# Kernel optimization log

Measured on AMD Instinct MI355X. Metric: run time of the kernel, lower is better.

## Reference

```python
import jax, jax.numpy as jnp
import numpy as np

DIM = 512
NUM_HEADS = 8
HEAD_DIM = DIM // NUM_HEADS          # 64
KEY_DIM = int(HEAD_DIM * 0.5)        # 32
H_QKV = DIM + NUM_HEADS * KEY_DIM * 2  # 1024
SCALE = KEY_DIM ** -0.5
EPS = 1e-5


def bn(x, gamma, beta, mean, var):
    # inference-mode BatchNorm2d over channel axis 1 of NCHW
    inv = gamma / jnp.sqrt(var + EPS)
    return x * inv[None, :, None, None] + (beta - mean * inv)[None, :, None, None]


def conv1x1(x, w):
    # w: [out, in] (1x1 conv collapsed); x: NCHW
    return jnp.einsum('bchw,oc->bohw', x, w)


def dwconv3x3(x, w):
    # depthwise 3x3, 'same' padding; w: [C,1,3,3]
    return jax.lax.conv_general_dilated(
        x, w, window_strides=(1, 1), padding='SAME',
        feature_group_count=x.shape[1],
        dimension_numbers=('NCHW', 'OIHW', 'NCHW'))


def setup_inputs() -> dict:
    key = jax.random.key(0)
    ks = jax.random.split(key, 16)
    B, C, H, W = 8, DIM, 40, 40
    f = jax.random.normal
    inp = {
        'x': f(ks[0], (B, C, H, W), jnp.float32),
        'qkv_w': f(ks[1], (H_QKV, DIM), jnp.float32) * (1.0 / np.sqrt(DIM)),
        'qkv_gamma': 1.0 + 0.1 * f(ks[2], (H_QKV,), jnp.float32),
        'qkv_beta': 0.1 * f(ks[3], (H_QKV,), jnp.float32),
        'qkv_mean': 0.1 * f(ks[4], (H_QKV,), jnp.float32),
        'qkv_var': jax.random.uniform(ks[5], (H_QKV,), jnp.float32) + 0.5,
        'pe_w': f(ks[6], (DIM, 1, 3, 3), jnp.float32) * (1.0 / 3.0),
        'pe_gamma': 1.0 + 0.1 * f(ks[7], (DIM,), jnp.float32),
        'pe_beta': 0.1 * f(ks[8], (DIM,), jnp.float32),
        'pe_mean': 0.1 * f(ks[9], (DIM,), jnp.float32),
        'pe_var': jax.random.uniform(ks[10], (DIM,), jnp.float32) + 0.5,
        'proj_w': f(ks[11], (DIM, DIM), jnp.float32) * (1.0 / np.sqrt(DIM)),
        'proj_gamma': 1.0 + 0.1 * f(ks[12], (DIM,), jnp.float32),
        'proj_beta': 0.1 * f(ks[13], (DIM,), jnp.float32),
        'proj_mean': 0.1 * f(ks[14], (DIM,), jnp.float32),
        'proj_var': jax.random.uniform(ks[15], (DIM,), jnp.float32) + 0.5,
    }
    return inp


def reference(x, qkv_w, qkv_gamma, qkv_beta, qkv_mean, qkv_var,
              pe_w, pe_gamma, pe_beta, pe_mean, pe_var,
              proj_w, proj_gamma, proj_beta, proj_mean, proj_var):
    B, C, H, W = x.shape
    N = H * W
    qkv = bn(conv1x1(x, qkv_w), qkv_gamma, qkv_beta, qkv_mean, qkv_var)
    qkv = qkv.reshape(B, NUM_HEADS, KEY_DIM * 2 + HEAD_DIM, N)
    q = qkv[:, :, :KEY_DIM]                    # [B,h,kd,N]
    k = qkv[:, :, KEY_DIM:2 * KEY_DIM]         # [B,h,kd,N]
    v = qkv[:, :, 2 * KEY_DIM:]                # [B,h,hd,N]
    # attn = q^T @ k * scale -> [B,h,N,N], softmax over last dim
    attn = jnp.einsum('bhkn,bhkm->bhnm', q, k) * SCALE
    attn = jax.nn.softmax(attn, axis=-1)
    # out = v @ attn^T -> [B,h,hd,N]
    out = jnp.einsum('bhdm,bhnm->bhdn', v, attn).reshape(B, C, H, W)
    pe = bn(dwconv3x3(v.reshape(B, C, H, W), pe_w), pe_gamma, pe_beta, pe_mean, pe_var)
    y = out + pe
    y = bn(conv1x1(y, proj_w), proj_gamma, proj_beta, proj_mean, proj_var)
    return y
```

## Files before the change

kernel.cpp:

```cpp
#include <hip/hip_runtime.h>
#include <hip/hip_bf16.h>

#define EPS 1e-5f
#define SCALE 0.17677669529663687f
#define QSCALE 0.25500526817095634f

typedef __attribute__((ext_vector_type(8))) short bf16x8;
typedef __attribute__((ext_vector_type(4))) float f32x4;
typedef __attribute__((ext_vector_type(8))) unsigned short u16x8;

__device__ __forceinline__ unsigned short f2bf(float x) {
  union { float f; unsigned int u; } a; a.f = x;
  unsigned int r = a.u + 0x7FFFu + ((a.u >> 16) & 1u);
  return (unsigned short)(r >> 16);
}
__device__ __forceinline__ float bf2f(unsigned short u) {
  union { unsigned int u; float f; } a; a.u = ((unsigned int)u) << 16;
  return a.f;
}

__device__ __forceinline__ float fexp2(float x) {
#if __has_builtin(__builtin_amdgcn_exp2f)
  return __builtin_amdgcn_exp2f(x);
#else
  float r; asm("v_exp_f32 %0, %1" : "=v"(r) : "v"(x)); return r;
#endif
}

__device__ __forceinline__ void gload_lds16(const void* g, void* l) {
  __builtin_amdgcn_global_load_lds(
      (const __attribute__((address_space(1))) unsigned int*)g,
      (__attribute__((address_space(3))) unsigned int*)l, 16, 0, 0);
}

__device__ __forceinline__ unsigned int pack_bf_trunc(float a, float b) {
  return __builtin_amdgcn_perm(__float_as_uint(b), __float_as_uint(a), 0x07060302u);
}

__global__ __launch_bounds__(256) void cast_w_kernel(
    const float* __restrict__ qw, const float* __restrict__ pw,
    short* __restrict__ wq, short* __restrict__ wp) {
  int idx = blockIdx.x * 256 + threadIdx.x;
  const float4* src;
  ushort4* dst;
  if (idx < 131072) {
    src = (const float4*)qw + idx;
    dst = (ushort4*)wq + idx;
  } else {
    src = (const float4*)pw + (idx - 131072);
    dst = (ushort4*)wp + (idx - 131072);
  }
  float4 v = *src;
  ushort4 u;
  u.x = f2bf(v.x); u.y = f2bf(v.y); u.z = f2bf(v.z); u.w = f2bf(v.w);
  *dst = u;
}

__global__ __launch_bounds__(256) void transpose_cast_kernel(
    const float* __restrict__ X, short* __restrict__ XT) {
  __shared__ unsigned short T[64][72];
  const int b = blockIdx.z, c0 = blockIdx.x * 64, n0 = blockIdx.y * 64;
  const int t = threadIdx.x, nl = t & 63, w = t >> 6;
#pragma unroll
  for (int ci = 0; ci < 16; ++ci) {
    int cl = ci * 4 + w;
    T[nl][cl] = f2bf(X[((size_t)(b * 512 + c0 + cl)) * 1600 + n0 + nl]);
  }
  __syncthreads();
  const int n2 = t >> 2, cg = (t & 3) * 16;
  unsigned short* o = (unsigned short*)XT + ((size_t)(b * 1600 + n0 + n2)) * 512 + c0 + cg;
  *(u16x8*)&o[0] = *(const u16x8*)&T[n2][cg];
  *(u16x8*)&o[8] = *(const u16x8*)&T[n2][cg + 8];
}

__global__ __launch_bounds__(256) void transpose16_kernel(
    const short* __restrict__ S, short* __restrict__ D) {
  __shared__ unsigned short T[64][72];
  const int b = blockIdx.z, c0 = blockIdx.x * 64, n0 = blockIdx.y * 64;
  const int t = threadIdx.x, nl = t & 63, w = t >> 6;
  const unsigned short* Sp = (const unsigned short*)S;
#pragma unroll
  for (int ci = 0; ci < 16; ++ci) {
    int cl = ci * 4 + w;
    T[nl][cl] = Sp[((size_t)(b * 512 + c0 + cl)) * 1600 + n0 + nl];
  }
  __syncthreads();
  const int n2 = t >> 2, cg = (t & 3) * 16;
  unsigned short* o = (unsigned short*)D + ((size_t)(b * 1600 + n0 + n2)) * 512 + c0 + cg;
  *(u16x8*)&o[0] = *(const u16x8*)&T[n2][cg];
  *(u16x8*)&o[8] = *(const u16x8*)&T[n2][cg + 8];
}

__global__ __launch_bounds__(256) void qkv_mfma_kernel(
    const short* __restrict__ XT, const short* __restrict__ WQ,
    const float* __restrict__ gamma, const float* __restrict__ beta,
    const float* __restrict__ mean, const float* __restrict__ var,
    short* __restrict__ qT, short* __restrict__ kT,
    short* __restrict__ vb, short* __restrict__ vp) {
  __shared__ __align__(16) unsigned short As[128 * 32];
  __shared__ __align__(16) unsigned short Bs[128 * 32];
  __shared__ __align__(16) unsigned short Vs[128 * 68];

  const int t = threadIdx.x, w = t >> 6, lane = t & 63;
  const int quad = lane >> 4, l16 = lane & 15;
  const int wr = w >> 1, wc = w & 1;
  const int ngt = blockIdx.x, h = blockIdx.y;
  const int o0 = h * 128, ng0 = ngt * 128;

  const int srow = lane >> 2;
  const int sseg = (lane & 3) * 8;

  f32x4 acc[4][4];
#pragma unroll
  for (int mi = 0; mi < 4; ++mi)
#pragma unroll
    for (int nj = 0; nj < 4; ++nj) { acc[mi][nj][0]=0.f; acc[mi][nj][1]=0.f; acc[mi][nj][2]=0.f; acc[mi][nj][3]=0.f; }

  for (int kt = 0; kt < 16; ++kt) {
    const int c0 = kt * 32;
    if (kt) __syncthreads();
#pragma unroll
    for (int r = 0; r < 2; ++r) {
      const int row = (r * 4 + w) * 16 + srow;
      gload_lds16(WQ + (size_t)(o0 + row) * 512 + c0 + sseg, As + (r * 4 + w) * 512);
      gload_lds16(XT + (size_t)(ng0 + row) * 512 + c0 + sseg, Bs + (r * 4 + w) * 512);
    }
    __syncthreads();
    bf16x8 af[4], bfr[4];
#pragma unroll
    for (int i = 0; i < 4; ++i) {
      af[i]  = *(const bf16x8*)&As[(wr * 64 + i * 16 + l16) * 32 + quad * 8];
      bfr[i] = *(const bf16x8*)&Bs[(wc * 64 + i * 16 + l16) * 32 + quad * 8];
    }
#pragma unroll
    for (int mi = 0; mi < 4; ++mi)
#pragma unroll
      for (int nj = 0; nj < 4; ++nj)
        acc[mi][nj] = __builtin_amdgcn_mfma_f32_16x16x32_bf16(af[mi], bfr[nj], acc[mi][nj], 0, 0, 0);
  }

  const int ng_base = ng0 + wc * 64;
#pragma unroll
  for (int mi = 0; mi < 4; ++mi) {
    const int ol = wr * 64 + mi * 16 + quad * 4;
    const int ob = o0 + ol;
    float inv[4], add[4];
#pragma unroll
    for (int r = 0; r < 4; ++r) {
      inv[r] = gamma[ob + r] * rsqrtf(var[ob + r] + EPS);
      add[r] = beta[ob + r] - mean[ob + r] * inv[r];
    }
    const int region = wr * 2 + (mi >> 1);
    if (region == 0) {
      const int kk = mi * 16 + quad * 4;
#pragma unroll
      for (int nj = 0; nj < 4; ++nj) {
        int ng = ng_base + nj * 16 + l16;
        int b = ng / 1600, n = ng - b * 1600;
        ushort4 u;
        u.x = f2bf((acc[mi][nj][0] * inv[0] + add[0]) * QSCALE);
        u.y = f2bf((acc[mi][nj][1] * inv[1] + add[1]) * QSCALE);
        u.z = f2bf((acc[mi][nj][2] * inv[2] + add[2]) * QSCALE);
        u.w = f2bf((acc[mi][nj][3] * inv[3] + add[3]) * QSCALE);
        *(ushort4*)&qT[((size_t)(b * 8 + h) * 1600 + n) * 32 + kk] = u;
      }
    } else if (region == 1) {
      const int kk = (mi - 2) * 16 + quad * 4;
#pragma unroll
      for (int nj = 0; nj < 4; ++nj) {
        int ng = ng_base + nj * 16 + l16;
        int b = ng / 1600, n = ng - b * 1600;
        ushort4 u;
        u.x = f2bf(acc[mi][nj][0] * inv[0] + add[0]);
        u.y = f2bf(acc[mi][nj][1] * inv[1] + add[1]);
        u.z = f2bf(acc[mi][nj][2] * inv[2] + add[2]);
        u.w = f2bf(acc[mi][nj][3] * inv[3] + add[3]);
        *(ushort4*)&kT[((size_t)(b * 8 + h) * 1600 + n) * 32 + kk] = u;
      }
    } else {
      const int ch = h * 64 + (ol - 64);
      const int d0 = ol - 64;
#pragma unroll
      for (int nj = 0; nj < 4; ++nj) {
        int ng = ng_base + nj * 16 + l16;
        int n_local = ng - ng0;
        int b = ng / 1600, n = ng - b * 1600;
        unsigned short val[4];
#pragma unroll
        for (int r = 0; r < 4; ++r)
          val[r] = f2bf(acc[mi][nj][r] * inv[r] + add[r]);
#pragma unroll
        for (int r = 0; r < 4; ++r)
          ((unsigned short*)vb)[((size_t)(b * 512 + ch + r)) * 1600 + n] = val[r];
#pragma unroll
        for (int k = 0; k < 2; ++k) {
          unsigned int pk = (unsigned int)val[2 * k] |
                            ((unsigned int)val[2 * k + 1] << 16);
          *(unsigned int*)&Vs[n_local * 68 + d0 + 2 * k] = pk;
        }
      }
    }
  }

  __syncthreads();
#pragma unroll
  for (int cc = 0; cc < 4; ++cc) {
    const int c = cc * 256 + t;
    const int kbl = c >> 6, d = c & 63;
    const int n_gl = ng0 + kbl * 8;
    const int b = n_gl / 1600, nn = n_gl - b * 1600;
    union { unsigned short u[8]; u16x8 v; } pk;
#pragma unroll
    for (int j = 0; j < 8; ++j)
      pk.u[j] = Vs[(kbl * 8 + j) * 68 + d];
    *(u16x8*)((unsigned short*)vp +
        ((size_t)(b * 8 + h) * 200 + (nn >> 3)) * 512 + d * 8) = pk.v;
  }
}

__global__ __launch_bounds__(256) void attn_mfma_kernel(
    const short* __restrict__ qT, const short* __restrict__ kT,
    const short* __restrict__ vp, short* __restrict__ ybf) {
  const int N = 1600;
  const int t = threadIdx.x;
  const int w = t >> 6, lane = t & 63, quad = lane >> 4, l16 = lane & 15;
  const int bh = blockIdx.x, b = bh >> 3, h = bh & 7;
  const int n0w = blockIdx.y * 128 + w * 32;
  if (n0w >= 1600) return;

  const unsigned short* qTb = (const unsigned short*)qT + (size_t)bh * N * 32;
  const unsigned short* kTb = (const unsigned short*)kT + (size_t)bh * N * 32;
  const unsigned short* vpb = (const unsigned short*)vp + (size_t)bh * 102400;

  const bf16x8 qf0 = *(const bf16x8*)(qTb + (size_t)(n0w + l16) * 32 + quad * 8);
  const bf16x8 qf1 = *(const bf16x8*)(qTb + (size_t)(n0w + 16 + l16) * 32 + quad * 8);

  f32x4 acc0[4], acc1[4];
#pragma unroll
  for (int i = 0; i < 4; ++i) {
    acc0[i][0]=0.f; acc0[i][1]=0.f; acc0[i][2]=0.f; acc0[i][3]=0.f;
    acc1[i][0]=0.f; acc1[i][1]=0.f; acc1[i][2]=0.f; acc1[i][3]=0.f;
  }
  float den0 = 0.f, den1 = 0.f;
  const f32x4 zero4 = {0.f, 0.f, 0.f, 0.f};

  const int kperm = ((l16 & 12) << 1) + (l16 & 3);
  const unsigned short* kp = kTb + (size_t)kperm * 32 + quad * 8;
  const unsigned short* vq = vpb + (size_t)quad * 512 + l16 * 8;

  bf16x8 ck0 = *(const bf16x8*)kp;
  bf16x8 ck1 = *(const bf16x8*)(kp + 128);
  bf16x8 cv0 = *(const bf16x8*)(vq);
  bf16x8 cv1 = *(const bf16x8*)(vq + 128);
  bf16x8 cv2 = *(const bf16x8*)(vq + 256);
  bf16x8 cv3 = *(const bf16x8*)(vq + 384);
  bf16x8 nk0, nk1, nv0, nv1, nv2, nv3;

#define ATTN_BODY(NXT, CK0, CK1, CV0, CV1, CV2, CV3, NK0, NK1, NV0, NV1, NV2, NV3) \
  { \
    const int nx_ = (NXT) < 50 ? (NXT) : 0; \
    const unsigned short* kpn_ = kp + (size_t)nx_ * 1024; \
    const unsigned short* vqn_ = vq + (size_t)nx_ * 2048; \
    NK0 = *(const bf16x8*)kpn_; \
    NK1 = *(const bf16x8*)(kpn_ + 128); \
    NV0 = *(const bf16x8*)(vqn_); \
    NV1 = *(const bf16x8*)(vqn_ + 128); \
    NV2 = *(const bf16x8*)(vqn_ + 256); \
    NV3 = *(const bf16x8*)(vqn_ + 384); \
    f32x4 s0_ = __builtin_amdgcn_mfma_f32_16x16x32_bf16(CK0, qf0, zero4, 0, 0, 0); \
    f32x4 s1_ = __builtin_amdgcn_mfma_f32_16x16x32_bf16(CK1, qf0, zero4, 0, 0, 0); \
    f32x4 t0_ = __builtin_amdgcn_mfma_f32_16x16x32_bf16(CK0, qf1, zero4, 0, 0, 0); \
    f32x4 t1_ = __builtin_amdgcn_mfma_f32_16x16x32_bf16(CK1, qf1, zero4, 0, 0, 0); \
    float a0_ = fexp2(s0_[0]), a1_ = fexp2(s0_[1]), a2_ = fexp2(s0_[2]), a3_ = fexp2(s0_[3]); \
    float a4_ = fexp2(s1_[0]), a5_ = fexp2(s1_[1]), a6_ = fexp2(s1_[2]), a7_ = fexp2(s1_[3]); \
    float b0_ = fexp2(t0_[0]), b1_ = fexp2(t0_[1]), b2_ = fexp2(t0_[2]), b3_ = fexp2(t0_[3]); \
    float b4_ = fexp2(t1_[0]), b5_ = fexp2(t1_[1]), b6_ = fexp2(t1_[2]), b7_ = fexp2(t1_[3]); \
    den0 += ((a0_ + a1_) + (a2_ + a3_)) + ((a4_ + a5_) + (a6_ + a7_)); \
    den1 += ((b0_ + b1_) + (b2_ + b3_)) + ((b4_ + b5_) + (b6_ + b7_)); \
    union { bf16x8 v; uint4 u; } pk0_, pk1_; \
    pk0_.u.x = pack_bf_trunc(a0_, a1_); pk0_.u.y = pack_bf_trunc(a2_, a3_); \
    pk0_.u.z = pack_bf_trunc(a4_, a5_); pk0_.u.w = pack_bf_trunc(a6_, a7_); \
    pk1_.u.x = pack_bf_trunc(b0_, b1_); pk1_.u.y = pack_bf_trunc(b2_, b3_); \
    pk1_.u.z = pack_bf_trunc(b4_, b5_); pk1_.u.w = pack_bf_trunc(b6_, b7_); \
    acc0[0] = __builtin_amdgcn_mfma_f32_16x16x32_bf16(pk0_.v, CV0, acc0[0], 0, 0, 0); \
    acc1[0] = __builtin_amdgcn_mfma_f32_16x16x32_bf16(pk1_.v, CV0, acc1[0], 0, 0, 0); \
    acc0[1] = __builtin_amdgcn_mfma_f32_16x16x32_bf16(pk0_.v, CV1, acc0[1], 0, 0, 0); \
    acc1[1] = __builtin_amdgcn_mfma_f32_16x16x32_bf16(pk1_.v, CV1, acc1[1], 0, 0, 0); \
    acc0[2] = __builtin_amdgcn_mfma_f32_16x16x32_bf16(pk0_.v, CV2, acc0[2], 0, 0, 0); \
    acc1[2] = __builtin_amdgcn_mfma_f32_16x16x32_bf16(pk1_.v, CV2, acc1[2], 0, 0, 0); \
    acc0[3] = __builtin_amdgcn_mfma_f32_16x16x32_bf16(pk0_.v, CV3, acc0[3], 0, 0, 0); \
    acc1[3] = __builtin_amdgcn_mfma_f32_16x16x32_bf16(pk1_.v, CV3, acc1[3], 0, 0, 0); \
  }

#pragma unroll 1
  for (int mt2 = 0; mt2 < 25; ++mt2) {
    ATTN_BODY(2 * mt2 + 1, ck0, ck1, cv0, cv1, cv2, cv3, nk0, nk1, nv0, nv1, nv2, nv3);
    ATTN_BODY(2 * mt2 + 2, nk0, nk1, nv0, nv1, nv2, nv3, ck0, ck1, cv0, cv1, cv2, cv3);
  }
#undef ATTN_BODY

  den0 += __shfl_xor(den0, 16, 64);
  den0 += __shfl_xor(den0, 32, 64);
  den1 += __shfl_xor(den1, 16, 64);
  den1 += __shfl_xor(den1, 32, 64);
  const float rden0 = 1.f / den0;
  const float rden1 = 1.f / den1;
  float dv0[4], dv1[4];
#pragma unroll
  for (int r = 0; r < 4; ++r) {
    dv0[r] = __shfl(rden0, quad * 4 + r, 64);
    dv1[r] = __shfl(rden1, quad * 4 + r, 64);
  }

  unsigned short* yb = (unsigned short*)ybf + ((size_t)b * 512 + h * 64) * N;
#pragma unroll
  for (int i = 0; i < 4; ++i) {
    const size_t rowo = (size_t)(i * 16 + l16) * N;
    ushort4 o4;
    o4.x = f2bf(acc0[i][0] * dv0[0]);
    o4.y = f2bf(acc0[i][1] * dv0[1]);
    o4.z = f2bf(acc0[i][2] * dv0[2]);
    o4.w = f2bf(acc0[i][3] * dv0[3]);
    *(ushort4*)&yb[rowo + n0w + quad * 4] = o4;
    o4.x = f2bf(acc1[i][0] * dv1[0]);
    o4.y = f2bf(acc1[i][1] * dv1[1]);
    o4.z = f2bf(acc1[i][2] * dv1[2]);
    o4.w = f2bf(acc1[i][3] * dv1[3]);
    *(ushort4*)&yb[rowo + n0w + 16 + quad * 4] = o4;
  }
}

__global__ __launch_bounds__(256) void pe_kernel(
    const short* __restrict__ Ybf, const short* __restrict__ VB,
    const float* __restrict__ pw,
    const float* __restrict__ gamma, const float* __restrict__ beta,
    const float* __restrict__ mean, const float* __restrict__ var,
    short* __restrict__ YB) {
  __shared__ __align__(16) unsigned short V[4 * 42 * 56];
  __shared__ float wlds[36];
  __shared__ float invs[4], adds[4];

  const int t = threadIdx.x;
  const int b = blockIdx.y, c0 = blockIdx.x * 4;

  const u16x8 z = {0, 0, 0, 0, 0, 0, 0, 0};
  for (int k = t; k < 1176; k += 256)
    *(u16x8*)&V[k * 8] = z;
  if (t < 36) wlds[t] = pw[c0 * 9 + t];
  if (t < 4) {
    int c = c0 + t;
    float inv = gamma[c] * rsqrtf(var[c] + EPS);
    invs[t] = inv;
    adds[t] = beta[c] - mean[c] * inv;
  }
  __syncthreads();

  for (int u = t; u < 800; u += 256) {
    int ch = u / 200, j = u - ch * 200;
    int row = j / 5, col8 = (j - row * 5) * 8;
    u16x8 d = *(const u16x8*)((const unsigned short*)VB +
        ((size_t)(b * 512 + c0 + ch) * 1600 + row * 40 + col8));
    *(u16x8*)&V[ch * 2352 + (row + 1) * 56 + 8 + col8] = d;
  }
  __syncthreads();

  for (int u = t; u < 800; u += 256) {
    int ch = u / 200, j = u - ch * 200;
    int row = j / 5, col8 = (j - row * 5) * 8;
    const unsigned short* Vc = &V[ch * 2352 + (row + 1) * 56 + 8 + col8];
    const float* wk = &wlds[ch * 9];
    float s[8];
#pragma unroll
    for (int jj = 0; jj < 8; ++jj) s[jj] = 0.f;
#pragma unroll
    for (int dy = 0; dy < 3; ++dy) {
      const unsigned short* Vr = Vc + (dy - 1) * 56;
      u16x8 cv = *(const u16x8*)Vr;
      float c[8];
#pragma unroll
      for (int jj = 0; jj < 8; ++jj) c[jj] = bf2f(cv[jj]);
      float left = bf2f(Vr[-1]);
      float right = bf2f(Vr[8]);
      const float w0 = wk[dy * 3 + 0], w1 = wk[dy * 3 + 1], w2 = wk[dy * 3 + 2];
      s[0] += w0 * left + w1 * c[0] + w2 * c[1];
#pragma unroll
      for (int jj = 1; jj < 7; ++jj)
        s[jj] += w0 * c[jj - 1] + w1 * c[jj] + w2 * c[jj + 1];
      s[7] += w0 * c[6] + w1 * c[7] + w2 * right;
    }
    size_t idx = (size_t)(b * 512 + c0 + ch) * 1600 + row * 40 + col8;
    u16x8 yv = *(const u16x8*)((const unsigned short*)Ybf + idx);
    union { unsigned short u[8]; u16x8 v; } o;
#pragma unroll
    for (int jj = 0; jj < 8; ++jj)
      o.u[jj] = f2bf(bf2f(yv[jj]) + s[jj] * invs[ch] + adds[ch]);
    *(u16x8*)((unsigned short*)YB + idx) = o.v;
  }
}

__global__ __launch_bounds__(256) void proj_mfma_kernel(
    const short* __restrict__ YT, const short* __restrict__ WP,
    const float* __restrict__ gamma, const float* __restrict__ beta,
    const float* __restrict__ mean, const float* __restrict__ var,
    float* __restrict__ OUT) {
  __shared__ __align__(16) unsigned short As[64 * 32];
  __shared__ __align__(16) unsigned short Bs[128 * 32];

  const int t = threadIdx.x, w = t >> 6, lane = t & 63;
  const int quad = lane >> 4, l16 = lane & 15;
  const int wr = w >> 1, wc = w & 1;
  const int ngt = blockIdx.x;
  const int o0 = blockIdx.y * 64;
  const int ng0 = ngt * 128;

  const int srow = lane >> 2;
  const int sseg = (lane & 3) * 8;

  f32x4 acc[2][4];
#pragma unroll
  for (int mi = 0; mi < 2; ++mi)
#pragma unroll
    for (int nj = 0; nj < 4; ++nj) { acc[mi][nj][0]=0.f; acc[mi][nj][1]=0.f; acc[mi][nj][2]=0.f; acc[mi][nj][3]=0.f; }

  for (int kt = 0; kt < 16; ++kt) {
    const int c0 = kt * 32;
    if (kt) __syncthreads();
    {
      const int row = w * 16 + srow;
      gload_lds16(WP + (size_t)(o0 + row) * 512 + c0 + sseg, As + w * 512);
    }
#pragma unroll
    for (int r = 0; r < 2; ++r) {
      const int row = (r * 4 + w) * 16 + srow;
      gload_lds16(YT + (size_t)(ng0 + row) * 512 + c0 + sseg, Bs + (r * 4 + w) * 512);
    }
    __syncthreads();
    bf16x8 af[2], bfr[4];
#pragma unroll
    for (int i = 0; i < 2; ++i)
      af[i] = *(const bf16x8*)&As[(wr * 32 + i * 16 + l16) * 32 + quad * 8];
#pragma unroll
    for (int i = 0; i < 4; ++i)
      bfr[i] = *(const bf16x8*)&Bs[(wc * 64 + i * 16 + l16) * 32 + quad * 8];
#pragma unroll
    for (int mi = 0; mi < 2; ++mi)
#pragma unroll
      for (int nj = 0; nj < 4; ++nj)
        acc[mi][nj] = __builtin_amdgcn_mfma_f32_16x16x32_bf16(af[mi], bfr[nj], acc[mi][nj], 0, 0, 0);
  }

  const int ng_base = ng0 + wc * 64;
#pragma unroll
  for (int mi = 0; mi < 2; ++mi) {
    const int ob = o0 + wr * 32 + mi * 16 + quad * 4;
    float inv[4], add[4];
#pragma unroll
    for (int r = 0; r < 4; ++r) {
      inv[r] = gamma[ob + r] * rsqrtf(var[ob + r] + EPS);
      add[r] = beta[ob + r] - mean[ob + r] * inv[r];
    }
#pragma unroll
    for (int nj = 0; nj < 4; ++nj) {
      int ng = ng_base + nj * 16 + l16;
      int b = ng / 1600, n = ng - b * 1600;
#pragma unroll
      for (int r = 0; r < 4; ++r)
        OUT[((size_t)(b * 512 + ob + r)) * 1600 + n] = acc[mi][nj][r] * inv[r] + add[r];
    }
  }
}

extern "C" void kernel_launch(void* const* d_in, const int* in_sizes, int n_in,
                              void* d_out, int out_size, void* d_ws, size_t ws_size,
                              hipStream_t stream) {
  const float* x          = (const float*)d_in[0];
  const float* qkv_w      = (const float*)d_in[1];
  const float* qkv_gamma  = (const float*)d_in[2];
  const float* qkv_beta   = (const float*)d_in[3];
  const float* qkv_mean   = (const float*)d_in[4];
  const float* qkv_var    = (const float*)d_in[5];
  const float* pe_w       = (const float*)d_in[6];
  const float* pe_gamma   = (const float*)d_in[7];
  const float* pe_beta    = (const float*)d_in[8];
  const float* pe_mean    = (const float*)d_in[9];
  const float* pe_var     = (const float*)d_in[10];
  const float* proj_w     = (const float*)d_in[11];
  const float* proj_gamma = (const float*)d_in[12];
  const float* proj_beta  = (const float*)d_in[13];
  const float* proj_mean  = (const float*)d_in[14];
  const float* proj_var   = (const float*)d_in[15];
  float* out = (float*)d_out;

  float* ws_a = (float*)d_ws;
  short* ybf_attn = (short*)d_ws;
  short* vp   = ybf_attn + (size_t)6553600;
  short* qT   = (short*)(ws_a + (size_t)6553600);
  short* kT   = qT + (size_t)3276800;
  short* vb   = kT + (size_t)3276800;
  short* xT   = vb + (size_t)6553600;
  short* wq   = xT + (size_t)6553600;
  short* wp   = wq + (size_t)524288;
  short* yT   = xT;
  short* ybf_pe = qT;

  cast_w_kernel<<<768, 256, 0, stream>>>(qkv_w, proj_w, wq, wp);
  {
    dim3 grid(8, 25, 8), block(256);
    transpose_cast_kernel<<<grid, block, 0, stream>>>(x, xT);
  }
  {
    dim3 grid(100, 8), block(256);
    qkv_mfma_kernel<<<grid, block, 0, stream>>>(
        xT, wq, qkv_gamma, qkv_beta, qkv_mean, qkv_var, qT, kT, vb, vp);
  }
  {
    dim3 grid(64, 13), block(256);
    attn_mfma_kernel<<<grid, block, 0, stream>>>(qT, kT, vp, ybf_attn);
  }
  {
    dim3 grid(128, 8), block(256);
    pe_kernel<<<grid, block, 0, stream>>>(
        ybf_attn, vb, pe_w, pe_gamma, pe_beta, pe_mean, pe_var, ybf_pe);
  }
  {
    dim3 grid(8, 25, 8), block(256);
    transpose16_kernel<<<grid, block, 0, stream>>>(ybf_pe, yT);
  }
  {
    dim3 grid(100, 8), block(256);
    proj_mfma_kernel<<<grid, block, 0, stream>>>(
        yT, wp, proj_gamma, proj_beta, proj_mean, proj_var, out);
  }
}
```

Measured before the change: 226.1 us.

## Fuse depthwise PE conv with transpose and read V from packed attention layout

```diff
diff --git a/kernel.cpp b/kernel.cpp
--- a/kernel.cpp
+++ b/kernel.cpp
@@ -73,30 +73,11 @@
   *(u16x8*)&o[8] = *(const u16x8*)&T[n2][cg + 8];
 }
 
-__global__ __launch_bounds__(256) void transpose16_kernel(
-    const short* __restrict__ S, short* __restrict__ D) {
-  __shared__ unsigned short T[64][72];
-  const int b = blockIdx.z, c0 = blockIdx.x * 64, n0 = blockIdx.y * 64;
-  const int t = threadIdx.x, nl = t & 63, w = t >> 6;
-  const unsigned short* Sp = (const unsigned short*)S;
-#pragma unroll
-  for (int ci = 0; ci < 16; ++ci) {
-    int cl = ci * 4 + w;
-    T[nl][cl] = Sp[((size_t)(b * 512 + c0 + cl)) * 1600 + n0 + nl];
-  }
-  __syncthreads();
-  const int n2 = t >> 2, cg = (t & 3) * 16;
-  unsigned short* o = (unsigned short*)D + ((size_t)(b * 1600 + n0 + n2)) * 512 + c0 + cg;
-  *(u16x8*)&o[0] = *(const u16x8*)&T[n2][cg];
-  *(u16x8*)&o[8] = *(const u16x8*)&T[n2][cg + 8];
-}
-
 __global__ __launch_bounds__(256) void qkv_mfma_kernel(
     const short* __restrict__ XT, const short* __restrict__ WQ,
     const float* __restrict__ gamma, const float* __restrict__ beta,
     const float* __restrict__ mean, const float* __restrict__ var,
-    short* __restrict__ qT, short* __restrict__ kT,
-    short* __restrict__ vb, short* __restrict__ vp) {
+    short* __restrict__ qT, short* __restrict__ kT, short* __restrict__ vp) {
   __shared__ __align__(16) unsigned short As[128 * 32];
   __shared__ __align__(16) unsigned short Bs[128 * 32];
   __shared__ __align__(16) unsigned short Vs[128 * 68];
@@ -178,20 +159,15 @@
         *(ushort4*)&kT[((size_t)(b * 8 + h) * 1600 + n) * 32 + kk] = u;
       }
     } else {
-      const int ch = h * 64 + (ol - 64);
       const int d0 = ol - 64;
 #pragma unroll
       for (int nj = 0; nj < 4; ++nj) {
         int ng = ng_base + nj * 16 + l16;
         int n_local = ng - ng0;
-        int b = ng / 1600, n = ng - b * 1600;
         unsigned short val[4];
 #pragma unroll
         for (int r = 0; r < 4; ++r)
           val[r] = f2bf(acc[mi][nj][r] * inv[r] + add[r]);
-#pragma unroll
-        for (int r = 0; r < 4; ++r)
-          ((unsigned short*)vb)[((size_t)(b * 512 + ch + r)) * 1600 + n] = val[r];
 #pragma unroll
         for (int k = 0; k < 2; ++k) {
           unsigned int pk = (unsigned int)val[2 * k] |
@@ -330,45 +306,50 @@
   }
 }
 
-__global__ __launch_bounds__(256) void pe_kernel(
-    const short* __restrict__ Ybf, const short* __restrict__ VB,
+__global__ __launch_bounds__(256) void pe_fused_kernel(
+    const short* __restrict__ Ybf, const short* __restrict__ VP,
     const float* __restrict__ pw,
     const float* __restrict__ gamma, const float* __restrict__ beta,
     const float* __restrict__ mean, const float* __restrict__ var,
-    short* __restrict__ YB) {
-  __shared__ __align__(16) unsigned short V[4 * 42 * 56];
-  __shared__ float wlds[36];
-  __shared__ float invs[4], adds[4];
+    short* __restrict__ YT) {
+  __shared__ __align__(16) unsigned short Vh[64 * 394];
+  __shared__ __align__(16) unsigned short Yt[64 * 208];
+  __shared__ float wlds[576];
+  __shared__ float invs[64], adds[64];
 
   const int t = threadIdx.x;
-  const int b = blockIdx.y, c0 = blockIdx.x * 4;
-
-  const u16x8 z = {0, 0, 0, 0, 0, 0, 0, 0};
-  for (int k = t; k < 1176; k += 256)
-    *(u16x8*)&V[k * 8] = z;
-  if (t < 36) wlds[t] = pw[c0 * 9 + t];
-  if (t < 4) {
+  const int h = blockIdx.x, nch = blockIdx.y, b = blockIdx.z;
+  const int c0 = h * 64, n0 = nch * 200, r0 = nch * 5;
+
+  for (int u = t; u < 576; u += 256) wlds[u] = pw[c0 * 9 + u];
+  if (t < 64) {
     int c = c0 + t;
     float inv = gamma[c] * rsqrtf(var[c] + EPS);
     invs[t] = inv;
     adds[t] = beta[c] - mean[c] * inv;
   }
+  const u16x8 z = {0, 0, 0, 0, 0, 0, 0, 0};
+  for (int k = t; k < 3152; k += 256)
+    *(u16x8*)&Vh[k * 8] = z;
   __syncthreads();
 
-  for (int u = t; u < 800; u += 256) {
-    int ch = u / 200, j = u - ch * 200;
-    int row = j / 5, col8 = (j - row * 5) * 8;
-    u16x8 d = *(const u16x8*)((const unsigned short*)VB +
-        ((size_t)(b * 512 + c0 + ch) * 1600 + row * 40 + col8));
-    *(u16x8*)&V[ch * 2352 + (row + 1) * 56 + 8 + col8] = d;
+  const unsigned short* vpb = (const unsigned short*)VP + (size_t)(b * 8 + h) * 102400;
+  for (int u = t; u < 2240; u += 256) {
+    const int d = u & 63, idx = u >> 6;
+    const int rl = idx / 5, cb = idx % 5;
+    const int rr = r0 - 1 + rl;
+    if (rr >= 0 && rr < 40) {
+      u16x8 ch8 = *(const u16x8*)(vpb + (size_t)(rr * 5 + cb) * 512 + d * 8);
+      *(u16x8*)&Vh[d * 394 + rl * 56 + 8 + cb * 8] = ch8;
+    }
   }
   __syncthreads();
 
-  for (int u = t; u < 800; u += 256) {
-    int ch = u / 200, j = u - ch * 200;
-    int row = j / 5, col8 = (j - row * 5) * 8;
-    const unsigned short* Vc = &V[ch * 2352 + (row + 1) * 56 + 8 + col8];
-    const float* wk = &wlds[ch * 9];
+  for (int u = t; u < 1600; u += 256) {
+    const int d = u / 25, seg = u % 25;
+    const int ry = seg / 5, cb8 = (seg % 5) * 8;
+    const unsigned short* Vc = &Vh[d * 394 + (ry + 1) * 56 + 8 + cb8];
+    const float* wk = &wlds[d * 9];
     float s[8];
 #pragma unroll
     for (int jj = 0; jj < 8; ++jj) s[jj] = 0.f;
@@ -388,13 +369,24 @@
         s[jj] += w0 * c[jj - 1] + w1 * c[jj] + w2 * c[jj + 1];
       s[7] += w0 * c[6] + w1 * c[7] + w2 * right;
     }
-    size_t idx = (size_t)(b * 512 + c0 + ch) * 1600 + row * 40 + col8;
+    const size_t idx = (size_t)(b * 512 + c0 + d) * 1600 + (r0 + ry) * 40 + cb8;
     u16x8 yv = *(const u16x8*)((const unsigned short*)Ybf + idx);
     union { unsigned short u[8]; u16x8 v; } o;
 #pragma unroll
     for (int jj = 0; jj < 8; ++jj)
-      o.u[jj] = f2bf(bf2f(yv[jj]) + s[jj] * invs[ch] + adds[ch]);
-    *(u16x8*)((unsigned short*)YB + idx) = o.v;
+      o.u[jj] = f2bf(bf2f(yv[jj]) + s[jj] * invs[d] + adds[d]);
+    *(u16x8*)&Yt[d * 208 + seg * 8] = o.v;
+  }
+  __syncthreads();
+
+  for (int u = t; u < 1600; u += 256) {
+    const int j = u >> 3, ds8 = u & 7;
+    union { unsigned short u[8]; u16x8 v; } o;
+#pragma unroll
+    for (int jj = 0; jj < 8; ++jj)
+      o.u[jj] = Yt[(ds8 * 8 + jj) * 208 + j];
+    *(u16x8*)((unsigned short*)YT +
+        ((size_t)(b * 1600 + n0 + j)) * 512 + c0 + ds8 * 8) = o.v;
   }
 }
 
@@ -496,12 +488,11 @@
   short* vp   = ybf_attn + (size_t)6553600;
   short* qT   = (short*)(ws_a + (size_t)6553600);
   short* kT   = qT + (size_t)3276800;
-  short* vb   = kT + (size_t)3276800;
-  short* xT   = vb + (size_t)6553600;
+  short* vb_unused = kT + (size_t)3276800;
+  short* xT   = vb_unused + (size_t)6553600;
   short* wq   = xT + (size_t)6553600;
   short* wp   = wq + (size_t)524288;
   short* yT   = xT;
-  short* ybf_pe = qT;
 
   cast_w_kernel<<<768, 256, 0, stream>>>(qkv_w, proj_w, wq, wp);
   {
@@ -511,20 +502,16 @@
   {
     dim3 grid(100, 8), block(256);
     qkv_mfma_kernel<<<grid, block, 0, stream>>>(
-        xT, wq, qkv_gamma, qkv_beta, qkv_mean, qkv_var, qT, kT, vb, vp);
+        xT, wq, qkv_gamma, qkv_beta, qkv_mean, qkv_var, qT, kT, vp);
   }
   {
     dim3 grid(64, 13), block(256);
     attn_mfma_kernel<<<grid, block, 0, stream>>>(qT, kT, vp, ybf_attn);
   }
   {
-    dim3 grid(128, 8), block(256);
-    pe_kernel<<<grid, block, 0, stream>>>(
-        ybf_attn, vb, pe_w, pe_gamma, pe_beta, pe_mean, pe_var, ybf_pe);
-  }
-  {
-    dim3 grid(8, 25, 8), block(256);
-    transpose16_kernel<<<grid, block, 0, stream>>>(ybf_pe, yT);
+    dim3 grid(8, 8, 8), block(256);
+    pe_fused_kernel<<<grid, block, 0, stream>>>(
+        ybf_attn, vp, pe_w, pe_gamma, pe_beta, pe_mean, pe_var, yT);
   }
   {
     dim3 grid(100, 8), block(256);
```

Measured after the change: 222.0 us. Within noise of the previous version (-1.8%).
